# Optimization experiments

Hardware: AMD Instinct MI355X
Metric: run time of the kernel (lower is better)

Reference implementation:

```python
import jax, jax.numpy as jnp
import numpy as np

N, D = 768, 128  # num_cells, gnn embedding dim (sum(gnn_layers_out_chnls))

def setup_inputs() -> dict:
    key = jax.random.key(0)
    ks = jax.random.split(key, 5)
    z = jax.random.normal(ks[0], (N, D), dtype=jnp.float32)
    W1 = jax.random.normal(ks[1], (256, 2 * D), dtype=jnp.float32) * 0.05
    b1 = jnp.zeros((256,), dtype=jnp.float32)
    W2 = jax.random.normal(ks[2], (128, 256), dtype=jnp.float32) * 0.05
    b2 = jnp.zeros((128,), dtype=jnp.float32)
    Wf = jax.random.normal(ks[3], (2, 128), dtype=jnp.float32) * 0.05
    bf = jnp.zeros((2,), dtype=jnp.float32)
    return {"z": z, "W1": W1, "b1": b1, "W2": W2, "b2": b2, "Wf": Wf, "bf": bf}

def reference(z, W1, b1, W2, b2, Wf, bf):
    # pairs[i, j] = concat(z[j], z[i])  (rtile varies over j, ctile over i)
    # First 1x1 conv over the 2D-channel pair tensor is equivalent to two
    # small matmuls broadcast-summed (same math, avoids N*N*2D materialization).
    d = z.shape[1]
    row_part = jnp.einsum('jd,od->jo', z, W1[:, :d])   # contribution of z[j]
    col_part = jnp.einsum('id,od->io', z, W1[:, d:])   # contribution of z[i]
    h = jax.nn.relu(row_part[None, :, :] + col_part[:, None, :] + b1)  # [N, N, 256]
    # dropout is identity in eval mode (training=False)
    h = jax.nn.relu(jnp.einsum('ijc,oc->ijo', h, W2) + b2)             # [N, N, 128]
    dists = jnp.einsum('ijc,oc->ijo', h, Wf) + bf                      # [N, N, 2]
    return dists
```

## Files before the change

### kernel.cpp

```cpp
#include <hip/hip_runtime.h>


typedef __attribute__((ext_vector_type(8)))  _Float16     f16x8;
typedef __attribute__((ext_vector_type(2)))  float        f32x2;
typedef __attribute__((ext_vector_type(4)))  float        f32x4;
typedef unsigned int u32;
typedef __attribute__((ext_vector_type(4)))  u32          u32x4;

#define NCELL 768
#define DIM   128
#define C1    256
#define C2    128

#define CPL    0
#define TABA   6144
#define TABB   7168
#define CBo    7680
#define LDS_SZ 19968

#define MFMA16(a, b, c) __builtin_amdgcn_mfma_f32_16x16x32_f16(a, b, c, 0, 0, 0)

static __device__ __forceinline__ u32 pk_add_f16(u32 a, u32 b) {
    u32 d; asm("v_pk_add_f16 %0, %1, %2" : "=v"(d) : "v"(a), "v"(b)); return d;
}
static __device__ __forceinline__ u32 pk_max_f16(u32 a, u32 b) {
    u32 d; asm("v_pk_max_f16 %0, %1, %2" : "=v"(d) : "v"(a), "v"(b)); return d;
}
static __device__ __forceinline__ f32x2 pk_add(f32x2 a, f32x2 b) {
    f32x2 d; asm("v_pk_add_f32 %0, %1, %2" : "=v"(d) : "v"(a), "v"(b)); return d;
}
static __device__ __forceinline__ f32x2 pk_fma(f32x2 a, f32x2 b, f32x2 c) {
    f32x2 d; asm("v_pk_fma_f32 %0, %1, %2, %3" : "=v"(d) : "v"(a), "v"(b), "v"(c)); return d;
}
static __device__ __forceinline__ f32x2 relu2(f32x2 a) {
    f32x2 d; d[0] = fmaxf(a[0], 0.f); d[1] = fmaxf(a[1], 0.f); return d;
}
static __device__ __forceinline__ f32x2 lo2(f32x4 v) { return __builtin_shufflevector(v, v, 0, 1); }
static __device__ __forceinline__ f32x2 hi2(f32x4 v) { return __builtin_shufflevector(v, v, 2, 3); }
static __device__ __forceinline__ f16x8 hgen(u32x4 rp, u32x4 cv, u32 zz) {
    u32x4 h;
#pragma unroll
    for (int w = 0; w < 4; ++w) h[w] = pk_max_f16(pk_add_f16(rp[w], cv[w]), zz);
    return __builtin_bit_cast(f16x8, h);
}

__global__ __launch_bounds__(256) void prep_all(const float* __restrict__ z,
                                                const float* __restrict__ W1,
                                                const float* __restrict__ b1,
                                                const float* __restrict__ W2,
                                                _Float16* __restrict__ rp16,
                                                _Float16* __restrict__ cp16,
                                                _Float16* __restrict__ w2h) {
    const int tid = threadIdx.x;
    if (blockIdx.x < 192) {
        const int jb4 = blockIdx.x * 4;
        __shared__ float zl[4 * DIM];
        zl[tid]       = z[(size_t)jb4 * DIM + tid];
        zl[tid + 256] = z[(size_t)jb4 * DIM + tid + 256];
        __syncthreads();
        const int o = tid;
        float a1[4] = {0.f, 0.f, 0.f, 0.f};
        float a2[4] = {0.f, 0.f, 0.f, 0.f};
        const f32x4* w4 = (const f32x4*)(W1 + (size_t)o * (2 * DIM));
#pragma unroll 4
        for (int d4 = 0; d4 < 32; ++d4) {
            f32x4 wa = w4[d4], wb = w4[32 + d4];
#pragma unroll
            for (int jj = 0; jj < 4; ++jj) {
                f32x4 zv = *(const f32x4*)(zl + jj * DIM + d4 * 4);
#pragma unroll
                for (int e = 0; e < 4; ++e) {
                    a1[jj] = fmaf(zv[e], wa[e], a1[jj]);
                    a2[jj] = fmaf(zv[e], wb[e], a2[jj]);
                }
            }
        }
        const float bb = b1[o];
#pragma unroll
        for (int jj = 0; jj < 4; ++jj) {
            rp16[(size_t)(jb4 + jj) * C1 + o] = (_Float16)(a1[jj] + bb);
            cp16[(size_t)(jb4 + jj) * C1 + o] = (_Float16)a2[jj];
        }
    } else {
        const int t = (blockIdx.x - 192) * 256 + tid;
        w2h[t] = (_Float16)W2[t];
    }
}

__global__ __launch_bounds__(256, 2) void pair_head(const _Float16* __restrict__ rp16,
                                                    const _Float16* __restrict__ cp16,
                                                    const _Float16* __restrict__ w2h,
                                                    const float* __restrict__ Wf,
                                                    const float* __restrict__ b2,
                                                    const float* __restrict__ bfv,
                                                    float* __restrict__ out) {
    __shared__ char smem[LDS_SZ];
    const int tid = threadIdx.x;
    const int nh  = tid >> 6;
    const int l   = tid & 63;
    const int lc  = l & 15;
    const int lg  = l >> 4;
    const int jbg = blockIdx.x >> 6;
    const int ic  = blockIdx.x & 63;
    const int j0  = jbg * 32;
    const int i_base = ic * 12;

#pragma unroll
    for (int q = 0; q < 6; ++q) {
        int off = q * 256 + tid;
        ((unsigned*)(smem + CPL))[off] =
            ((const unsigned*)(cp16 + (size_t)i_base * C1))[off];
    }
    if (tid < 64) {
        int n0 = 2 * tid;
        f32x4 A = {b2[n0], b2[n0 + 1], Wf[n0], Wf[n0 + 1]};
        f32x2 B = {Wf[C2 + n0], Wf[C2 + n0 + 1]};
        *(f32x4*)(smem + TABA + tid * 16) = A;
        *(f32x2*)(smem + TABB + tid * 8)  = B;
    }

    u32x4 rpf[2][8];
#pragma unroll
    for (int jh = 0; jh < 2; ++jh)
#pragma unroll
        for (int ks = 0; ks < 8; ++ks)
            rpf[jh][ks] = *(const u32x4*)(rp16 + (size_t)(j0 + jh * 16 + lc) * C1 + lg * 8 + ks * 32);

    f16x8 w2f[2][8];
#pragma unroll
    for (int ng = 0; ng < 2; ++ng)
#pragma unroll
        for (int ks = 0; ks < 8; ++ks)
            w2f[ng][ks] = *(const f16x8*)(w2h + (size_t)(nh * 32 + ng * 16 + lc) * C1 + lg * 8 + ks * 32);

    __syncthreads();

    const u32 zz = 0;

    for (int t = 0; t < 6; ++t) {
        const char* c0 = smem + CPL + (2 * t) * 512 + lg * 16;

        f32x4 ac[2][4];
#pragma unroll
        for (int g = 0; g < 2; ++g)
#pragma unroll
            for (int c = 0; c < 4; ++c) ac[g][c] = (f32x4)0.f;

#pragma unroll
        for (int ks = 0; ks < 8; ++ks) {
            u32x4 cv0 = *(const u32x4*)(c0 + ks * 64);
            u32x4 cv1 = *(const u32x4*)(c0 + 512 + ks * 64);
            f16x8 hb;
            hb = hgen(rpf[0][ks], cv0, zz);
            ac[0][0] = MFMA16(w2f[0][ks], hb, ac[0][0]);
            ac[1][0] = MFMA16(w2f[1][ks], hb, ac[1][0]);
            hb = hgen(rpf[1][ks], cv0, zz);
            ac[0][1] = MFMA16(w2f[0][ks], hb, ac[0][1]);
            ac[1][1] = MFMA16(w2f[1][ks], hb, ac[1][1]);
            hb = hgen(rpf[0][ks], cv1, zz);
            ac[0][2] = MFMA16(w2f[0][ks], hb, ac[0][2]);
            ac[1][2] = MFMA16(w2f[1][ks], hb, ac[1][2]);
            hb = hgen(rpf[1][ks], cv1, zz);
            ac[0][3] = MFMA16(w2f[0][ks], hb, ac[0][3]);
            ac[1][3] = MFMA16(w2f[1][ks], hb, ac[1][3]);
        }

        f32x2 P0[4], P1[4];
#pragma unroll
        for (int c = 0; c < 4; ++c) { P0[c] = (f32x2){0.f, 0.f}; P1[c] = (f32x2){0.f, 0.f}; }
#pragma unroll
        for (int ng = 0; ng < 2; ++ng) {
#pragma unroll
            for (int rp2 = 0; rp2 < 2; ++rp2) {
                int np = nh * 16 + ng * 8 + lg * 2 + rp2;
                f32x4 A = *(const f32x4*)(smem + TABA + np * 16);
                f32x2 B = *(const f32x2*)(smem + TABB + np * 8);
#pragma unroll
                for (int c = 0; c < 4; ++c) {
                    f32x2 s = {ac[ng][c][2 * rp2], ac[ng][c][2 * rp2 + 1]};
                    s = relu2(pk_add(s, lo2(A)));
                    P0[c] = pk_fma(hi2(A), s, P0[c]);
                    P1[c] = pk_fma(B, s, P1[c]);
                }
            }
        }
#pragma unroll
        for (int c = 0; c < 4; ++c) {
            float p0 = P0[c][0] + P0[c][1];
            float p1 = P1[c][0] + P1[c][1];
            p0 += __shfl_xor(p0, 16); p1 += __shfl_xor(p1, 16);
            p0 += __shfl_xor(p0, 32); p1 += __shfl_xor(p1, 32);
            if (l < 16) {
                int p = t * 64 + (c >> 1) * 32 + (c & 1) * 16 + l;
                *(f32x2*)(smem + CBo + nh * 3072 + p * 8) = (f32x2){p0, p1};
            }
        }
    }

    __syncthreads();

    const float bf0 = bfv[0], bf1 = bfv[1];
#pragma unroll
    for (int p = tid; p < 384; p += 256) {
        f32x2 a0 = *(const f32x2*)(smem + CBo +        p * 8);
        f32x2 a1 = *(const f32x2*)(smem + CBo + 3072 + p * 8);
        f32x2 a2 = *(const f32x2*)(smem + CBo + 6144 + p * 8);
        f32x2 a3 = *(const f32x2*)(smem + CBo + 9216 + p * 8);
        float o0 = a0[0] + a1[0] + a2[0] + a3[0] + bf0;
        float o1 = a0[1] + a1[1] + a2[1] + a3[1] + bf1;
        int c = p & 15, jh = (p >> 4) & 1, ii = (p >> 5) & 1, t = p >> 6;
        int i = i_base + 2 * t + ii;
        int j = j0 + jh * 16 + c;
        *(f32x2*)(out + ((size_t)i * NCELL + j) * 2) = (f32x2){o0, o1};
    }
}

extern "C" void kernel_launch(void* const* d_in, const int* in_sizes, int n_in,
                              void* d_out, int out_size, void* d_ws, size_t ws_size,
                              hipStream_t stream) {
    const float* z   = (const float*)d_in[0];
    const float* W1  = (const float*)d_in[1];
    const float* b1  = (const float*)d_in[2];
    const float* W2  = (const float*)d_in[3];
    const float* b2  = (const float*)d_in[4];
    const float* Wf  = (const float*)d_in[5];
    const float* bfv = (const float*)d_in[6];
    float* out = (float*)d_out;

    _Float16* rp16 = (_Float16*)d_ws;
    _Float16* cp16 = rp16 + NCELL * C1;
    _Float16* w2h  = cp16 + NCELL * C1;

    prep_all<<<192 + 128, 256, 0, stream>>>(z, W1, b1, W2, rp16, cp16, w2h);
    pair_head<<<24 * 64, 256, 0, stream>>>(rp16, cp16, w2h, Wf, b2, bfv, out);
}
```

Measured before the change: 68.76 us.

## Halve per-block j tile to cut registers and double blocks per CU

The pair_head kernel now covers 16 j columns per block instead of 32. This halves the rp fragment and accumulator registers, shrinks the LDS partial-sum buffer, raises launch bounds to 4 blocks per CU and doubles the grid. The inline-asm packed f16 add/max is replaced by vector-type elementwise add and max, and the t loop is no longer unrolled. The cost is that each cp tile and the W2 fragments are reloaded twice as often, and each h vector now feeds fewer MFMAs.

```diff
diff --git a/kernel.cpp b/kernel.cpp
--- a/kernel.cpp
+++ b/kernel.cpp
@@ -1,11 +1,9 @@
 #include <hip/hip_runtime.h>
 
 
-typedef __attribute__((ext_vector_type(8)))  _Float16     f16x8;
-typedef __attribute__((ext_vector_type(2)))  float        f32x2;
-typedef __attribute__((ext_vector_type(4)))  float        f32x4;
-typedef unsigned int u32;
-typedef __attribute__((ext_vector_type(4)))  u32          u32x4;
+typedef __attribute__((ext_vector_type(8)))  _Float16 f16x8;
+typedef __attribute__((ext_vector_type(2)))  float    f32x2;
+typedef __attribute__((ext_vector_type(4)))  float    f32x4;
 
 #define NCELL 768
 #define DIM   128
@@ -16,16 +14,10 @@
 #define TABA   6144
 #define TABB   7168
 #define CBo    7680
-#define LDS_SZ 19968
+#define LDS_SZ 13824
 
 #define MFMA16(a, b, c) __builtin_amdgcn_mfma_f32_16x16x32_f16(a, b, c, 0, 0, 0)
 
-static __device__ __forceinline__ u32 pk_add_f16(u32 a, u32 b) {
-    u32 d; asm("v_pk_add_f16 %0, %1, %2" : "=v"(d) : "v"(a), "v"(b)); return d;
-}
-static __device__ __forceinline__ u32 pk_max_f16(u32 a, u32 b) {
-    u32 d; asm("v_pk_max_f16 %0, %1, %2" : "=v"(d) : "v"(a), "v"(b)); return d;
-}
 static __device__ __forceinline__ f32x2 pk_add(f32x2 a, f32x2 b) {
     f32x2 d; asm("v_pk_add_f32 %0, %1, %2" : "=v"(d) : "v"(a), "v"(b)); return d;
 }
@@ -37,12 +29,6 @@
 }
 static __device__ __forceinline__ f32x2 lo2(f32x4 v) { return __builtin_shufflevector(v, v, 0, 1); }
 static __device__ __forceinline__ f32x2 hi2(f32x4 v) { return __builtin_shufflevector(v, v, 2, 3); }
-static __device__ __forceinline__ f16x8 hgen(u32x4 rp, u32x4 cv, u32 zz) {
-    u32x4 h;
-#pragma unroll
-    for (int w = 0; w < 4; ++w) h[w] = pk_max_f16(pk_add_f16(rp[w], cv[w]), zz);
-    return __builtin_bit_cast(f16x8, h);
-}
 
 __global__ __launch_bounds__(256) void prep_all(const float* __restrict__ z,
                                                 const float* __restrict__ W1,
@@ -87,7 +73,7 @@
     }
 }
 
-__global__ __launch_bounds__(256, 2) void pair_head(const _Float16* __restrict__ rp16,
+__global__ __launch_bounds__(256, 4) void pair_head(const _Float16* __restrict__ rp16,
                                                     const _Float16* __restrict__ cp16,
                                                     const _Float16* __restrict__ w2h,
                                                     const float* __restrict__ Wf,
@@ -102,7 +88,7 @@
     const int lg  = l >> 4;
     const int jbg = blockIdx.x >> 6;
     const int ic  = blockIdx.x & 63;
-    const int j0  = jbg * 32;
+    const int j0  = jbg * 16;
     const int i_base = ic * 12;
 
 #pragma unroll
@@ -119,12 +105,10 @@
         *(f32x2*)(smem + TABB + tid * 8)  = B;
     }
 
-    u32x4 rpf[2][8];
-#pragma unroll
-    for (int jh = 0; jh < 2; ++jh)
-#pragma unroll
-        for (int ks = 0; ks < 8; ++ks)
-            rpf[jh][ks] = *(const u32x4*)(rp16 + (size_t)(j0 + jh * 16 + lc) * C1 + lg * 8 + ks * 32);
+    f16x8 rpf[8];
+#pragma unroll
+    for (int ks = 0; ks < 8; ++ks)
+        rpf[ks] = *(const f16x8*)(rp16 + (size_t)(j0 + lc) * C1 + lg * 8 + ks * 32);
 
     f16x8 w2f[2][8];
 #pragma unroll
@@ -135,39 +119,33 @@
 
     __syncthreads();
 
-    const u32 zz = 0;
-
+    const f16x8 z8 = (f16x8)(_Float16)0.0f;
+
+#pragma unroll 1
     for (int t = 0; t < 6; ++t) {
         const char* c0 = smem + CPL + (2 * t) * 512 + lg * 16;
 
-        f32x4 ac[2][4];
+        f32x4 ac[2][2];
 #pragma unroll
         for (int g = 0; g < 2; ++g)
 #pragma unroll
-            for (int c = 0; c < 4; ++c) ac[g][c] = (f32x4)0.f;
+            for (int c = 0; c < 2; ++c) ac[g][c] = (f32x4)0.f;
 
 #pragma unroll
         for (int ks = 0; ks < 8; ++ks) {
-            u32x4 cv0 = *(const u32x4*)(c0 + ks * 64);
-            u32x4 cv1 = *(const u32x4*)(c0 + 512 + ks * 64);
-            f16x8 hb;
-            hb = hgen(rpf[0][ks], cv0, zz);
-            ac[0][0] = MFMA16(w2f[0][ks], hb, ac[0][0]);
-            ac[1][0] = MFMA16(w2f[1][ks], hb, ac[1][0]);
-            hb = hgen(rpf[1][ks], cv0, zz);
-            ac[0][1] = MFMA16(w2f[0][ks], hb, ac[0][1]);
-            ac[1][1] = MFMA16(w2f[1][ks], hb, ac[1][1]);
-            hb = hgen(rpf[0][ks], cv1, zz);
-            ac[0][2] = MFMA16(w2f[0][ks], hb, ac[0][2]);
-            ac[1][2] = MFMA16(w2f[1][ks], hb, ac[1][2]);
-            hb = hgen(rpf[1][ks], cv1, zz);
-            ac[0][3] = MFMA16(w2f[0][ks], hb, ac[0][3]);
-            ac[1][3] = MFMA16(w2f[1][ks], hb, ac[1][3]);
-        }
-
-        f32x2 P0[4], P1[4];
-#pragma unroll
-        for (int c = 0; c < 4; ++c) { P0[c] = (f32x2){0.f, 0.f}; P1[c] = (f32x2){0.f, 0.f}; }
+            f16x8 cv0 = *(const f16x8*)(c0 + ks * 64);
+            f16x8 cv1 = *(const f16x8*)(c0 + 512 + ks * 64);
+            f16x8 hb0 = __builtin_elementwise_max(rpf[ks] + cv0, z8);
+            ac[0][0] = MFMA16(w2f[0][ks], hb0, ac[0][0]);
+            ac[1][0] = MFMA16(w2f[1][ks], hb0, ac[1][0]);
+            f16x8 hb1 = __builtin_elementwise_max(rpf[ks] + cv1, z8);
+            ac[0][1] = MFMA16(w2f[0][ks], hb1, ac[0][1]);
+            ac[1][1] = MFMA16(w2f[1][ks], hb1, ac[1][1]);
+        }
+
+        f32x2 P0[2], P1[2];
+#pragma unroll
+        for (int c = 0; c < 2; ++c) { P0[c] = (f32x2){0.f, 0.f}; P1[c] = (f32x2){0.f, 0.f}; }
 #pragma unroll
         for (int ng = 0; ng < 2; ++ng) {
 #pragma unroll
@@ -176,7 +154,7 @@
                 f32x4 A = *(const f32x4*)(smem + TABA + np * 16);
                 f32x2 B = *(const f32x2*)(smem + TABB + np * 8);
 #pragma unroll
-                for (int c = 0; c < 4; ++c) {
+                for (int c = 0; c < 2; ++c) {
                     f32x2 s = {ac[ng][c][2 * rp2], ac[ng][c][2 * rp2 + 1]};
                     s = relu2(pk_add(s, lo2(A)));
                     P0[c] = pk_fma(hi2(A), s, P0[c]);
@@ -185,14 +163,14 @@
             }
         }
 #pragma unroll
-        for (int c = 0; c < 4; ++c) {
+        for (int c = 0; c < 2; ++c) {
             float p0 = P0[c][0] + P0[c][1];
             float p1 = P1[c][0] + P1[c][1];
             p0 += __shfl_xor(p0, 16); p1 += __shfl_xor(p1, 16);
             p0 += __shfl_xor(p0, 32); p1 += __shfl_xor(p1, 32);
             if (l < 16) {
-                int p = t * 64 + (c >> 1) * 32 + (c & 1) * 16 + l;
-                *(f32x2*)(smem + CBo + nh * 3072 + p * 8) = (f32x2){p0, p1};
+                int p = t * 32 + c * 16 + l;
+                *(f32x2*)(smem + CBo + nh * 1536 + p * 8) = (f32x2){p0, p1};
             }
         }
     }
@@ -200,17 +178,17 @@
     __syncthreads();
 
     const float bf0 = bfv[0], bf1 = bfv[1];
-#pragma unroll
-    for (int p = tid; p < 384; p += 256) {
+    if (tid < 192) {
+        const int p = tid;
         f32x2 a0 = *(const f32x2*)(smem + CBo +        p * 8);
-        f32x2 a1 = *(const f32x2*)(smem + CBo + 3072 + p * 8);
-        f32x2 a2 = *(const f32x2*)(smem + CBo + 6144 + p * 8);
-        f32x2 a3 = *(const f32x2*)(smem + CBo + 9216 + p * 8);
+        f32x2 a1 = *(const f32x2*)(smem + CBo + 1536 + p * 8);
+        f32x2 a2 = *(const f32x2*)(smem + CBo + 3072 + p * 8);
+        f32x2 a3 = *(const f32x2*)(smem + CBo + 4608 + p * 8);
         float o0 = a0[0] + a1[0] + a2[0] + a3[0] + bf0;
         float o1 = a0[1] + a1[1] + a2[1] + a3[1] + bf1;
-        int c = p & 15, jh = (p >> 4) & 1, ii = (p >> 5) & 1, t = p >> 6;
+        int c = p & 15, ii = (p >> 4) & 1, t = p >> 5;
         int i = i_base + 2 * t + ii;
-        int j = j0 + jh * 16 + c;
+        int j = j0 + c;
         *(f32x2*)(out + ((size_t)i * NCELL + j) * 2) = (f32x2){o0, o1};
     }
 }
@@ -232,5 +210,5 @@
     _Float16* w2h  = cp16 + NCELL * C1;
 
     prep_all<<<192 + 128, 256, 0, stream>>>(z, W1, b1, W2, rp16, cp16, w2h);
-    pair_head<<<24 * 64, 256, 0, stream>>>(rp16, cp16, w2h, Wf, b2, bfv, out);
-}
+    pair_head<<<48 * 64, 256, 0, stream>>>(rp16, cp16, w2h, Wf, b2, bfv, out);
+}
```

Measured after the change: 84.09 us. 22.3% more time.
